# Optimization experiments

Measured on AMD Instinct MI355X. Metric: run time of the kernel, lower is better.

The kernel has to match this reference:

```python
import jax, jax.numpy as jnp
import numpy as np

QK_I2_S = 128  # elements per packed block (32 bytes -> 128 2-bit weights)


def unpack_weights_simd(packed):
    """Unpack SIMD block-interleaved 2-bit ternary weights.

    packed: (M, K//4) int values in [0, 256). Per 32-byte block, byte j holds
    weights at offsets j+0 (bits 6:7), j+32 (bits 4:5), j+64 (bits 2:3), j+96 (bits 0:1).
    Returns float32 (M, K) with values in {-1, 0, 1, 2}-1 = {-1,0,1,2}? (2-bit code minus 1).
    """
    M, Kp = packed.shape
    nb = Kp // 32                      # number of 128-element blocks
    p = packed.reshape(M, nb, 32)
    shifts = jnp.array([6, 4, 2, 0], dtype=jnp.int32)
    # (M, nb, 4, 32): axis 2 indexes the offset group {0,32,64,96}
    w = ((p[:, :, None, :] >> shifts[None, None, :, None]) & 3).astype(jnp.float32) - 1.0
    return w.reshape(M, nb * QK_I2_S)  # (M, K)


def quantize_activations_i8(x):
    """Per-token symmetric int8 quantization (absmax -> [-128, 127])."""
    absmax = jnp.max(jnp.abs(x), axis=-1, keepdims=True)
    q_scale = 127.0 / jnp.clip(absmax, 1e-5, None)   # x_i8 = round(x * q_scale)
    x_i8 = jnp.clip(jnp.round(x * q_scale), -128.0, 127.0)
    act_scale = 1.0 / q_scale                         # dequant scale = absmax/127
    return x_i8, act_scale


def setup_inputs() -> dict:
    key = jax.random.key(0)
    k1, k2, k3 = jax.random.split(key, 3)
    x = jax.random.normal(k1, (2, 2048, 4096), dtype=jnp.float32)
    weight = jax.random.randint(k2, (12288, 1024), 0, 256, dtype=jnp.int32)
    weight_scale = jax.random.uniform(k3, (1,), dtype=jnp.float32, minval=0.01, maxval=0.1)
    return {"x": x, "weight": weight, "weight_scale": weight_scale}


def reference(x, weight, weight_scale):
    orig_shape = x.shape[:-1]
    K = x.shape[-1]
    x_flat = x.reshape(-1, K).astype(jnp.float32)
    x_i8, act_scale = quantize_activations_i8(x_flat)      # (N,K), (N,1)
    W = unpack_weights_simd(weight)                         # (M,K) ternary-coded floats
    # bitnet_gemm: int8 activations x ternary weights, fused weight scale
    out = jnp.einsum('nk,mk->nm', x_i8, W) * weight_scale[0]
    out = (out * act_scale).astype(x.dtype)                 # dequantize activations
    return out.reshape(*orig_shape, -1)
```

## Files before the change

kernel.cpp:

```cpp
#include <hip/hip_runtime.h>

#define K_DIM 4096
#define M_DIM 12288
#define KW (K_DIM / 4)
#define NT_K (K_DIM / 128)
#define BM 256
#define BN 256
#define GN 16
#define GM 48

typedef __attribute__((ext_vector_type(4))) int i32x4;
typedef __attribute__((ext_vector_type(4))) unsigned int u32x4;

__device__ __forceinline__ int quant1(float v, float qs) {
  float r = rintf(v * qs);
  r = fminf(127.f, fmaxf(-128.f, r));
  return (int)r;
}

__device__ __forceinline__ unsigned int unp(unsigned int uv) {
  return ((uv >> 6) | (uv << 4) | (uv << 14) | (uv << 24)) & 0x03030303u;
}

__global__ __launch_bounds__(256) void quant_kernel(const float* __restrict__ x,
                                                    unsigned int* __restrict__ xq,
                                                    float2* __restrict__ scales) {
  const int n = blockIdx.x;
  const int t = threadIdx.x;
  const float* __restrict__ row = x + (size_t)n * K_DIM;
  const float4* __restrict__ row4 = (const float4*)row;

  float am = 0.f;
#pragma unroll
  for (int p = 0; p < 4; ++p) {
    float4 v = row4[t + 256 * p];
    am = fmaxf(am, fmaxf(fmaxf(fabsf(v.x), fabsf(v.y)), fmaxf(fabsf(v.z), fabsf(v.w))));
  }
#pragma unroll
  for (int off = 32; off; off >>= 1) am = fmaxf(am, __shfl_xor(am, off, 64));
  __shared__ float redf[4];
  __shared__ int redi[4];
  const int wave = t >> 6, lane = t & 63;
  if (lane == 0) redf[wave] = am;
  __syncthreads();
  am = fmaxf(fmaxf(redf[0], redf[1]), fmaxf(redf[2], redf[3]));
  const float clipped = fmaxf(am, 1e-5f);
  const float qs = 127.0f / clipped;

  int rsum = 0;
#pragma unroll
  for (int p = 0; p < 4; ++p) {
    const int w = t + 256 * p;
    const int b = w >> 5, j = w & 31;
    const int base = b * 128 + j;
    const int q0 = quant1(row[base], qs);
    const int q1 = quant1(row[base + 32], qs);
    const int q2 = quant1(row[base + 64], qs);
    const int q3 = quant1(row[base + 96], qs);
    rsum += q0 + q1 + q2 + q3;
    xq[(size_t)n * KW + w] = (unsigned int)(q0 & 255) | ((unsigned int)(q1 & 255) << 8) |
                             ((unsigned int)(q2 & 255) << 16) | ((unsigned int)(q3 & 255) << 24);
  }
#pragma unroll
  for (int off = 32; off; off >>= 1) rsum += __shfl_xor(rsum, off, 64);
  if (lane == 0) redi[wave] = rsum;
  __syncthreads();
  if (t == 0)
    scales[n] = make_float2(clipped * (1.0f / 127.0f),
                            (float)(redi[0] + redi[1] + redi[2] + redi[3]));
}

__global__ __launch_bounds__(256) void unpack_kernel(const i32x4* __restrict__ in,
                                                     u32x4* __restrict__ outp, int n4) {
  int idx = blockIdx.x * 256 + threadIdx.x;
  const int stride = gridDim.x * 256;
  for (; idx < n4; idx += stride) {
    i32x4 v = in[idx];
    u32x4 u = {unp((unsigned int)v[0]), unp((unsigned int)v[1]),
               unp((unsigned int)v[2]), unp((unsigned int)v[3])};
    outp[idx] = u;
  }
}

template <bool PRE>
__global__ __launch_bounds__(512) void bitgemm256(const unsigned char* __restrict__ xq,
                                                  const unsigned char* __restrict__ wu,
                                                  const int* __restrict__ wp,
                                                  const float2* __restrict__ scales,
                                                  const float* __restrict__ wsp,
                                                  float* __restrict__ out) {
  __shared__ __align__(16) unsigned char lds[131072];
  unsigned char* AsB = lds;
  unsigned char* BsB = lds + 65536;

  const int tid = threadIdx.x;
  const int l = tid & 63;
  const int w = tid >> 6;
  const int wm = w >> 2;
  const int wn = w & 3;

  const int cpx = gridDim.x >> 3;
  const int swz = (blockIdx.x & 7) * cpx + (blockIdx.x >> 3);
  const int bn = swz & (GN - 1);
  const int bm = swz >> 4;

  const int srow = tid >> 3;
  const int schunk = (tid & 7) ^ (srow & 7);
  const size_t soff = (size_t)srow * K_DIM + (schunk << 4);
  const unsigned char* aSrc = xq + (size_t)(bn * BM) * K_DIM + soff;
  const unsigned char* bSrc = wu + (size_t)(bm * BN) * K_DIM + soff;
  const int ldsDst = tid * 16;

  const int prow = tid >> 1, phalf = tid & 1;
  const int* pSrc = wp + (size_t)(bm * BN + prow) * KW + phalf * 16;
  const int pchunkbase = phalf * 4;
  const int pswz = prow & 7;
  const int pdst = prow * 128;

  int aoff[8], boff[4];
#pragma unroll
  for (int i = 0; i < 8; ++i) {
    const int r = wm * 128 + i * 16 + (l & 15);
    aoff[i] = r * 128 + (((l >> 4) ^ (r & 7)) << 4);
  }
#pragma unroll
  for (int j = 0; j < 4; ++j) {
    const int r = wn * 64 + j * 16 + (l & 15);
    boff[j] = r * 128 + (((l >> 4) ^ (r & 7)) << 4);
  }

  i32x4 acc[8][4];
#pragma unroll
  for (int i = 0; i < 8; ++i)
#pragma unroll
    for (int j = 0; j < 4; ++j) acc[i][j] = (i32x4){0, 0, 0, 0};

  auto stage = [&](int buf, int kb) {
    const int koff = kb * 128;
    unsigned char* ad = AsB + buf * 32768 + ldsDst;
    const unsigned char* as_ = aSrc + koff;
#pragma unroll
    for (int q = 0; q < 4; ++q)
      __builtin_amdgcn_global_load_lds(
          (const __attribute__((address_space(1))) void*)(as_ + (size_t)q * 64 * K_DIM),
          (__attribute__((address_space(3))) void*)(ad + q * 8192), 16, 0, 0);
    if (PRE) {
      unsigned char* bd = BsB + buf * 32768 + ldsDst;
      const unsigned char* bs_ = bSrc + koff;
#pragma unroll
      for (int q = 0; q < 4; ++q)
        __builtin_amdgcn_global_load_lds(
            (const __attribute__((address_space(1))) void*)(bs_ + (size_t)q * 64 * K_DIM),
            (__attribute__((address_space(3))) void*)(bd + q * 8192), 16, 0, 0);
    } else {
      const int* ps = pSrc + kb * 32;
      unsigned char* bd = BsB + buf * 32768 + pdst;
#pragma unroll
      for (int q = 0; q < 4; ++q) {
        i32x4 v = *(const i32x4*)(ps + q * 4);
        u32x4 u = {unp((unsigned int)v[0]), unp((unsigned int)v[1]),
                   unp((unsigned int)v[2]), unp((unsigned int)v[3])};
        *(u32x4*)(bd + (((pchunkbase + q) ^ pswz) << 4)) = u;
      }
    }
  };

  stage(0, 0);
  for (int kb = 0; kb < NT_K; ++kb) {
    const int cur = kb & 1;
    if (kb + 1 < NT_K) {
      stage(cur ^ 1, kb + 1);
      asm volatile("s_waitcnt vmcnt(8)" ::: "memory");
    } else {
      asm volatile("s_waitcnt vmcnt(0)" ::: "memory");
    }
    __builtin_amdgcn_s_barrier();

    const unsigned char* Ab = AsB + cur * 32768;
    const unsigned char* Bb = BsB + cur * 32768;
#pragma unroll
    for (int ks = 0; ks < 2; ++ks) {
      const int k6 = ks << 6;
      i32x4 af[8], bf[4];
#pragma unroll
      for (int i = 0; i < 8; ++i) af[i] = *(const i32x4*)(Ab + (aoff[i] ^ k6));
#pragma unroll
      for (int j = 0; j < 4; ++j) bf[j] = *(const i32x4*)(Bb + (boff[j] ^ k6));
      __builtin_amdgcn_s_setprio(1);
#pragma unroll
      for (int i = 0; i < 8; ++i)
#pragma unroll
        for (int j = 0; j < 4; ++j)
          acc[i][j] = __builtin_amdgcn_mfma_i32_16x16x64_i8(af[i], bf[j], acc[i][j], 0, 0, 0);
      __builtin_amdgcn_s_setprio(0);
    }
    if (!PRE) asm volatile("s_waitcnt lgkmcnt(0)" ::: "memory");
    __builtin_amdgcn_s_barrier();
  }

  const float wsc = wsp[0];
#pragma unroll
  for (int i = 0; i < 8; ++i) {
#pragma unroll
    for (int r = 0; r < 4; ++r) {
      const int n = bn * BM + wm * 128 + i * 16 + ((l >> 4) << 2) + r;
      const float2 sc = scales[n];
      const float f = wsc * sc.x;
      float* orow = out + (size_t)n * M_DIM + bm * BN + wn * 64 + (l & 15);
#pragma unroll
      for (int j = 0; j < 4; ++j) orow[j * 16] = ((float)acc[i][j][r] - sc.y) * f;
    }
  }
}

extern "C" void kernel_launch(void* const* d_in, const int* in_sizes, int n_in,
                              void* d_out, int out_size, void* d_ws, size_t ws_size,
                              hipStream_t stream) {
  const float* x = (const float*)d_in[0];
  const int* wp = (const int*)d_in[1];
  const float* wsp = (const float*)d_in[2];
  float* out = (float*)d_out;
  const int N = in_sizes[0] / K_DIM;

  float2* scales = (float2*)d_ws;
  unsigned int* xq = (unsigned int*)((char*)d_ws + 32768);
  const size_t xq_bytes = (size_t)N * KW * 4;
  unsigned char* wu = (unsigned char*)d_ws + 32768 + xq_bytes;
  const size_t need = 32768 + xq_bytes + (size_t)M_DIM * K_DIM;

  quant_kernel<<<N, 256, 0, stream>>>(x, xq, scales);
  const int grid = (N / BM) * GM;
  if (ws_size >= need) {
    unpack_kernel<<<2048, 256, 0, stream>>>((const i32x4*)wp, (u32x4*)wu, M_DIM * KW / 4);
    bitgemm256<true><<<grid, 512, 0, stream>>>((const unsigned char*)xq, wu, wp, scales, wsp, out);
  } else {
    bitgemm256<false><<<grid, 512, 0, stream>>>((const unsigned char*)xq, nullptr, wp, scales, wsp, out);
  }
}
```

Baseline: 237.6 us.

## Pre-tile unpacked weights in MFMA fragment order and load B directly to registers

Measured after the change: 254.9 us. 7.3% more time.

```diff
diff --git a/kernel.cpp b/kernel.cpp
--- a/kernel.cpp
+++ b/kernel.cpp
@@ -70,28 +70,53 @@
                             (float)(redi[0] + redi[1] + redi[2] + redi[3]));
 }
 
-__global__ __launch_bounds__(256) void unpack_kernel(const i32x4* __restrict__ in,
-                                                     u32x4* __restrict__ outp, int n4) {
-  int idx = blockIdx.x * 256 + threadIdx.x;
+__global__ __launch_bounds__(256) void unpack_tiled(const int* __restrict__ in,
+                                                    u32x4* __restrict__ outp) {
+  const int total = M_DIM * 256;
+  int t = blockIdx.x * 256 + threadIdx.x;
   const int stride = gridDim.x * 256;
-  for (; idx < n4; idx += stride) {
-    i32x4 v = in[idx];
-    u32x4 u = {unp((unsigned int)v[0]), unp((unsigned int)v[1]),
-               unp((unsigned int)v[2]), unp((unsigned int)v[3])};
-    outp[idx] = u;
-  }
-}
-
-template <bool PRE>
-__global__ __launch_bounds__(512) void bitgemm256(const unsigned char* __restrict__ xq,
-                                                  const unsigned char* __restrict__ wu,
-                                                  const int* __restrict__ wp,
-                                                  const float2* __restrict__ scales,
-                                                  const float* __restrict__ wsp,
-                                                  float* __restrict__ out) {
-  __shared__ __align__(16) unsigned char lds[131072];
-  unsigned char* AsB = lds;
-  unsigned char* BsB = lds + 65536;
+  for (; t < total; t += stride) {
+    const int lo = t & 15;
+    const int cc = (t >> 4) & 255;
+    const int rt = t >> 12;
+    const int r = rt * 16 + lo;
+    const i32x4 v = *(const i32x4*)(in + (size_t)r * KW + cc * 4);
+    u32x4 u = {unp((unsigned int)v[0]), unp((unsigned int)v[1]), unp((unsigned int)v[2]),
+               unp((unsigned int)v[3])};
+    const int kb = cc >> 3, c8 = cc & 7;
+    outp[rt * 4096 + kb * 128 + (c8 >> 2) * 64 + (c8 & 3) * 16 + lo] = u;
+  }
+}
+
+#define LOAD_B(dst, kb)                                                                   \
+  {                                                                                       \
+    _Pragma("unroll") for (int q_ = 0; q_ < 8; ++q_) dst[q_] =                            \
+        *(const i32x4*)(bBase + (q_ & 3) * 65536 + (q_ >> 2) * 1024 + (size_t)(kb) * 2048); \
+  }
+
+#define COMPUTE(Ab, bS)                                                                   \
+  {                                                                                       \
+    _Pragma("unroll") for (int ih_ = 0; ih_ < 2; ++ih_) {                                 \
+      _Pragma("unroll") for (int ks_ = 0; ks_ < 2; ++ks_) {                               \
+        i32x4 af[4];                                                                      \
+        _Pragma("unroll") for (int i_ = 0; i_ < 4; ++i_) af[i_] =                         \
+            *(const i32x4*)((Ab) + (aoff[ih_ * 4 + i_] ^ (ks_ << 6)));                    \
+        __builtin_amdgcn_s_setprio(1);                                                    \
+        _Pragma("unroll") for (int i_ = 0; i_ < 4; ++i_)                                  \
+            _Pragma("unroll") for (int j_ = 0; j_ < 4; ++j_) acc[ih_ * 4 + i_][j_] =      \
+                __builtin_amdgcn_mfma_i32_16x16x64_i8(af[i_], bS[ks_ * 4 + j_],           \
+                                                      acc[ih_ * 4 + i_][j_], 0, 0, 0);    \
+        __builtin_amdgcn_s_setprio(0);                                                    \
+      }                                                                                   \
+    }                                                                                     \
+  }
+
+__global__ __launch_bounds__(512, 2) void bitgemm256(const unsigned char* __restrict__ xq,
+                                                     const unsigned char* __restrict__ wu2,
+                                                     const float2* __restrict__ scales,
+                                                     const float* __restrict__ wsp,
+                                                     float* __restrict__ out) {
+  __shared__ __align__(16) unsigned char lds[65536];
 
   const int tid = threadIdx.x;
   const int l = tid & 63;
@@ -106,28 +131,17 @@
 
   const int srow = tid >> 3;
   const int schunk = (tid & 7) ^ (srow & 7);
-  const size_t soff = (size_t)srow * K_DIM + (schunk << 4);
-  const unsigned char* aSrc = xq + (size_t)(bn * BM) * K_DIM + soff;
-  const unsigned char* bSrc = wu + (size_t)(bm * BN) * K_DIM + soff;
+  const unsigned char* aSrc = xq + (size_t)(bn * BM) * K_DIM + (size_t)srow * K_DIM + (schunk << 4);
   const int ldsDst = tid * 16;
 
-  const int prow = tid >> 1, phalf = tid & 1;
-  const int* pSrc = wp + (size_t)(bm * BN + prow) * KW + phalf * 16;
-  const int pchunkbase = phalf * 4;
-  const int pswz = prow & 7;
-  const int pdst = prow * 128;
-
-  int aoff[8], boff[4];
+  const unsigned char* bBase = wu2 + (((size_t)(bm * 16 + wn * 4) * 4096 + l) << 4);
+
+  int aoff[8];
 #pragma unroll
   for (int i = 0; i < 8; ++i) {
     const int r = wm * 128 + i * 16 + (l & 15);
     aoff[i] = r * 128 + (((l >> 4) ^ (r & 7)) << 4);
   }
-#pragma unroll
-  for (int j = 0; j < 4; ++j) {
-    const int r = wn * 64 + j * 16 + (l & 15);
-    boff[j] = r * 128 + (((l >> 4) ^ (r & 7)) << 4);
-  }
 
   i32x4 acc[8][4];
 #pragma unroll
@@ -135,66 +149,39 @@
 #pragma unroll
     for (int j = 0; j < 4; ++j) acc[i][j] = (i32x4){0, 0, 0, 0};
 
-  auto stage = [&](int buf, int kb) {
-    const int koff = kb * 128;
-    unsigned char* ad = AsB + buf * 32768 + ldsDst;
-    const unsigned char* as_ = aSrc + koff;
+  auto stageA = [&](int buf, int kb) {
+    unsigned char* ad = lds + buf * 32768 + ldsDst;
+    const unsigned char* as_ = aSrc + kb * 128;
 #pragma unroll
     for (int q = 0; q < 4; ++q)
       __builtin_amdgcn_global_load_lds(
           (const __attribute__((address_space(1))) void*)(as_ + (size_t)q * 64 * K_DIM),
           (__attribute__((address_space(3))) void*)(ad + q * 8192), 16, 0, 0);
-    if (PRE) {
-      unsigned char* bd = BsB + buf * 32768 + ldsDst;
-      const unsigned char* bs_ = bSrc + koff;
-#pragma unroll
-      for (int q = 0; q < 4; ++q)
-        __builtin_amdgcn_global_load_lds(
-            (const __attribute__((address_space(1))) void*)(bs_ + (size_t)q * 64 * K_DIM),
-            (__attribute__((address_space(3))) void*)(bd + q * 8192), 16, 0, 0);
-    } else {
-      const int* ps = pSrc + kb * 32;
-      unsigned char* bd = BsB + buf * 32768 + pdst;
-#pragma unroll
-      for (int q = 0; q < 4; ++q) {
-        i32x4 v = *(const i32x4*)(ps + q * 4);
-        u32x4 u = {unp((unsigned int)v[0]), unp((unsigned int)v[1]),
-                   unp((unsigned int)v[2]), unp((unsigned int)v[3])};
-        *(u32x4*)(bd + (((pchunkbase + q) ^ pswz) << 4)) = u;
-      }
-    }
   };
 
-  stage(0, 0);
-  for (int kb = 0; kb < NT_K; ++kb) {
-    const int cur = kb & 1;
-    if (kb + 1 < NT_K) {
-      stage(cur ^ 1, kb + 1);
-      asm volatile("s_waitcnt vmcnt(8)" ::: "memory");
+  i32x4 bX[8], bY[8];
+  const unsigned char* A0 = lds;
+  const unsigned char* A1 = lds + 32768;
+
+  stageA(0, 0);
+  LOAD_B(bX, 0);
+  for (int kb2 = 0; kb2 < NT_K / 2; ++kb2) {
+    const int e = kb2 * 2;
+    stageA(1, e + 1);
+    LOAD_B(bY, e + 1);
+    asm volatile("s_waitcnt vmcnt(12)" ::: "memory");
+    __builtin_amdgcn_s_barrier();
+    COMPUTE(A0, bX);
+    __builtin_amdgcn_s_barrier();
+    if (kb2 < NT_K / 2 - 1) {
+      stageA(0, e + 2);
+      LOAD_B(bX, e + 2);
+      asm volatile("s_waitcnt vmcnt(12)" ::: "memory");
     } else {
       asm volatile("s_waitcnt vmcnt(0)" ::: "memory");
     }
     __builtin_amdgcn_s_barrier();
-
-    const unsigned char* Ab = AsB + cur * 32768;
-    const unsigned char* Bb = BsB + cur * 32768;
-#pragma unroll
-    for (int ks = 0; ks < 2; ++ks) {
-      const int k6 = ks << 6;
-      i32x4 af[8], bf[4];
-#pragma unroll
-      for (int i = 0; i < 8; ++i) af[i] = *(const i32x4*)(Ab + (aoff[i] ^ k6));
-#pragma unroll
-      for (int j = 0; j < 4; ++j) bf[j] = *(const i32x4*)(Bb + (boff[j] ^ k6));
-      __builtin_amdgcn_s_setprio(1);
-#pragma unroll
-      for (int i = 0; i < 8; ++i)
-#pragma unroll
-        for (int j = 0; j < 4; ++j)
-          acc[i][j] = __builtin_amdgcn_mfma_i32_16x16x64_i8(af[i], bf[j], acc[i][j], 0, 0, 0);
-      __builtin_amdgcn_s_setprio(0);
-    }
-    if (!PRE) asm volatile("s_waitcnt lgkmcnt(0)" ::: "memory");
+    COMPUTE(A1, bY);
     __builtin_amdgcn_s_barrier();
   }
 
@@ -225,15 +212,10 @@
   float2* scales = (float2*)d_ws;
   unsigned int* xq = (unsigned int*)((char*)d_ws + 32768);
   const size_t xq_bytes = (size_t)N * KW * 4;
-  unsigned char* wu = (unsigned char*)d_ws + 32768 + xq_bytes;
-  const size_t need = 32768 + xq_bytes + (size_t)M_DIM * K_DIM;
+  unsigned char* wu2 = (unsigned char*)d_ws + 32768 + xq_bytes;
 
   quant_kernel<<<N, 256, 0, stream>>>(x, xq, scales);
+  unpack_tiled<<<4096, 256, 0, stream>>>(wp, (u32x4*)wu2);
   const int grid = (N / BM) * GM;
-  if (ws_size >= need) {
-    unpack_kernel<<<2048, 256, 0, stream>>>((const i32x4*)wp, (u32x4*)wu, M_DIM * KW / 4);
-    bitgemm256<true><<<grid, 512, 0, stream>>>((const unsigned char*)xq, wu, wp, scales, wsp, out);
-  } else {
-    bitgemm256<false><<<grid, 512, 0, stream>>>((const unsigned char*)xq, nullptr, wp, scales, wsp, out);
-  }
-}
+  bitgemm256<<<grid, 512, 0, stream>>>((const unsigned char*)xq, wu2, scales, wsp, out);
+}
```

## Switch GEMM to 128x128 tiles with 4 waves and two blocks per CU

Applied to the files above, without the earlier changes.

After: 308.8 us. 30.0% more time.

```diff
diff --git a/kernel.cpp b/kernel.cpp
--- a/kernel.cpp
+++ b/kernel.cpp
@@ -4,10 +4,9 @@
 #define M_DIM 12288
 #define KW (K_DIM / 4)
 #define NT_K (K_DIM / 128)
-#define BM 256
-#define BN 256
-#define GN 16
-#define GM 48
+#define BT 128
+#define GN2 32
+#define GM2 96
 
 typedef __attribute__((ext_vector_type(4))) int i32x4;
 typedef __attribute__((ext_vector_type(4))) unsigned int u32x4;
@@ -82,86 +81,59 @@
   }
 }
 
-template <bool PRE>
-__global__ __launch_bounds__(512) void bitgemm256(const unsigned char* __restrict__ xq,
-                                                  const unsigned char* __restrict__ wu,
-                                                  const int* __restrict__ wp,
-                                                  const float2* __restrict__ scales,
-                                                  const float* __restrict__ wsp,
-                                                  float* __restrict__ out) {
-  __shared__ __align__(16) unsigned char lds[131072];
-  unsigned char* AsB = lds;
-  unsigned char* BsB = lds + 65536;
+__global__ __launch_bounds__(256, 2) void bitgemm128(const unsigned char* __restrict__ xq,
+                                                     const unsigned char* __restrict__ wu,
+                                                     const float2* __restrict__ scales,
+                                                     const float* __restrict__ wsp,
+                                                     float* __restrict__ out) {
+  __shared__ __align__(16) unsigned char lds[65536];
 
   const int tid = threadIdx.x;
   const int l = tid & 63;
   const int w = tid >> 6;
-  const int wm = w >> 2;
-  const int wn = w & 3;
+  const int wm = w >> 1;
+  const int wn = w & 1;
 
   const int cpx = gridDim.x >> 3;
   const int swz = (blockIdx.x & 7) * cpx + (blockIdx.x >> 3);
-  const int bn = swz & (GN - 1);
-  const int bm = swz >> 4;
+  const int bn = swz / GM2;
+  const int bm = swz % GM2;
 
   const int srow = tid >> 3;
   const int schunk = (tid & 7) ^ (srow & 7);
   const size_t soff = (size_t)srow * K_DIM + (schunk << 4);
-  const unsigned char* aSrc = xq + (size_t)(bn * BM) * K_DIM + soff;
-  const unsigned char* bSrc = wu + (size_t)(bm * BN) * K_DIM + soff;
+  const unsigned char* aSrc = xq + (size_t)(bn * BT) * K_DIM + soff;
+  const unsigned char* bSrc = wu + (size_t)(bm * BT) * K_DIM + soff;
   const int ldsDst = tid * 16;
 
-  const int prow = tid >> 1, phalf = tid & 1;
-  const int* pSrc = wp + (size_t)(bm * BN + prow) * KW + phalf * 16;
-  const int pchunkbase = phalf * 4;
-  const int pswz = prow & 7;
-  const int pdst = prow * 128;
-
-  int aoff[8], boff[4];
-#pragma unroll
-  for (int i = 0; i < 8; ++i) {
-    const int r = wm * 128 + i * 16 + (l & 15);
-    aoff[i] = r * 128 + (((l >> 4) ^ (r & 7)) << 4);
-  }
-#pragma unroll
-  for (int j = 0; j < 4; ++j) {
-    const int r = wn * 64 + j * 16 + (l & 15);
-    boff[j] = r * 128 + (((l >> 4) ^ (r & 7)) << 4);
-  }
-
-  i32x4 acc[8][4];
-#pragma unroll
-  for (int i = 0; i < 8; ++i)
+  int aoff[4], boff[4];
+#pragma unroll
+  for (int i = 0; i < 4; ++i) {
+    const int ra = wm * 64 + i * 16 + (l & 15);
+    aoff[i] = ra * 128 + (((l >> 4) ^ (ra & 7)) << 4);
+    const int rb = wn * 64 + i * 16 + (l & 15);
+    boff[i] = rb * 128 + (((l >> 4) ^ (rb & 7)) << 4);
+  }
+
+  i32x4 acc[4][4];
+#pragma unroll
+  for (int i = 0; i < 4; ++i)
 #pragma unroll
     for (int j = 0; j < 4; ++j) acc[i][j] = (i32x4){0, 0, 0, 0};
 
   auto stage = [&](int buf, int kb) {
-    const int koff = kb * 128;
-    unsigned char* ad = AsB + buf * 32768 + ldsDst;
-    const unsigned char* as_ = aSrc + koff;
-#pragma unroll
-    for (int q = 0; q < 4; ++q)
+    unsigned char* ad = lds + buf * 16384 + ldsDst;
+    unsigned char* bd = lds + 32768 + buf * 16384 + ldsDst;
+    const unsigned char* as_ = aSrc + kb * 128;
+    const unsigned char* bs_ = bSrc + kb * 128;
+#pragma unroll
+    for (int q = 0; q < 4; ++q) {
       __builtin_amdgcn_global_load_lds(
-          (const __attribute__((address_space(1))) void*)(as_ + (size_t)q * 64 * K_DIM),
-          (__attribute__((address_space(3))) void*)(ad + q * 8192), 16, 0, 0);
-    if (PRE) {
-      unsigned char* bd = BsB + buf * 32768 + ldsDst;
-      const unsigned char* bs_ = bSrc + koff;
-#pragma unroll
-      for (int q = 0; q < 4; ++q)
-        __builtin_amdgcn_global_load_lds(
-            (const __attribute__((address_space(1))) void*)(bs_ + (size_t)q * 64 * K_DIM),
-            (__attribute__((address_space(3))) void*)(bd + q * 8192), 16, 0, 0);
-    } else {
-      const int* ps = pSrc + kb * 32;
-      unsigned char* bd = BsB + buf * 32768 + pdst;
-#pragma unroll
-      for (int q = 0; q < 4; ++q) {
-        i32x4 v = *(const i32x4*)(ps + q * 4);
-        u32x4 u = {unp((unsigned int)v[0]), unp((unsigned int)v[1]),
-                   unp((unsigned int)v[2]), unp((unsigned int)v[3])};
-        *(u32x4*)(bd + (((pchunkbase + q) ^ pswz) << 4)) = u;
-      }
+          (const __attribute__((address_space(1))) void*)(as_ + (size_t)q * 32 * K_DIM),
+          (__attribute__((address_space(3))) void*)(ad + q * 4096), 16, 0, 0);
+      __builtin_amdgcn_global_load_lds(
+          (const __attribute__((address_space(1))) void*)(bs_ + (size_t)q * 32 * K_DIM),
+          (__attribute__((address_space(3))) void*)(bd + q * 4096), 16, 0, 0);
     }
   };
 
@@ -176,37 +148,39 @@
     }
     __builtin_amdgcn_s_barrier();
 
-    const unsigned char* Ab = AsB + cur * 32768;
-    const unsigned char* Bb = BsB + cur * 32768;
+    const unsigned char* Ab = lds + cur * 16384;
+    const unsigned char* Bb = lds + 32768 + cur * 16384;
+    i32x4 af[8], bf[8];
 #pragma unroll
     for (int ks = 0; ks < 2; ++ks) {
-      const int k6 = ks << 6;
-      i32x4 af[8], bf[4];
-#pragma unroll
-      for (int i = 0; i < 8; ++i) af[i] = *(const i32x4*)(Ab + (aoff[i] ^ k6));
-#pragma unroll
-      for (int j = 0; j < 4; ++j) bf[j] = *(const i32x4*)(Bb + (boff[j] ^ k6));
-      __builtin_amdgcn_s_setprio(1);
-#pragma unroll
-      for (int i = 0; i < 8; ++i)
+#pragma unroll
+      for (int i = 0; i < 4; ++i) {
+        af[ks * 4 + i] = *(const i32x4*)(Ab + (aoff[i] ^ (ks << 6)));
+        bf[ks * 4 + i] = *(const i32x4*)(Bb + (boff[i] ^ (ks << 6)));
+      }
+    }
+    __builtin_amdgcn_s_setprio(1);
+#pragma unroll
+    for (int ks = 0; ks < 2; ++ks)
+#pragma unroll
+      for (int i = 0; i < 4; ++i)
 #pragma unroll
         for (int j = 0; j < 4; ++j)
-          acc[i][j] = __builtin_amdgcn_mfma_i32_16x16x64_i8(af[i], bf[j], acc[i][j], 0, 0, 0);
-      __builtin_amdgcn_s_setprio(0);
-    }
-    if (!PRE) asm volatile("s_waitcnt lgkmcnt(0)" ::: "memory");
+          acc[i][j] = __builtin_amdgcn_mfma_i32_16x16x64_i8(af[ks * 4 + i], bf[ks * 4 + j],
+                                                            acc[i][j], 0, 0, 0);
+    __builtin_amdgcn_s_setprio(0);
     __builtin_amdgcn_s_barrier();
   }
 
   const float wsc = wsp[0];
 #pragma unroll
-  for (int i = 0; i < 8; ++i) {
+  for (int i = 0; i < 4; ++i) {
 #pragma unroll
     for (int r = 0; r < 4; ++r) {
-      const int n = bn * BM + wm * 128 + i * 16 + ((l >> 4) << 2) + r;
+      const int n = bn * BT + wm * 64 + i * 16 + ((l >> 4) << 2) + r;
       const float2 sc = scales[n];
       const float f = wsc * sc.x;
-      float* orow = out + (size_t)n * M_DIM + bm * BN + wn * 64 + (l & 15);
+      float* orow = out + (size_t)n * M_DIM + bm * BT + wn * 64 + (l & 15);
 #pragma unroll
       for (int j = 0; j < 4; ++j) orow[j * 16] = ((float)acc[i][j][r] - sc.y) * f;
     }
@@ -226,14 +200,9 @@
   unsigned int* xq = (unsigned int*)((char*)d_ws + 32768);
   const size_t xq_bytes = (size_t)N * KW * 4;
   unsigned char* wu = (unsigned char*)d_ws + 32768 + xq_bytes;
-  const size_t need = 32768 + xq_bytes + (size_t)M_DIM * K_DIM;
 
   quant_kernel<<<N, 256, 0, stream>>>(x, xq, scales);
-  const int grid = (N / BM) * GM;
-  if (ws_size >= need) {
-    unpack_kernel<<<2048, 256, 0, stream>>>((const i32x4*)wp, (u32x4*)wu, M_DIM * KW / 4);
-    bitgemm256<true><<<grid, 512, 0, stream>>>((const unsigned char*)xq, wu, wp, scales, wsp, out);
-  } else {
-    bitgemm256<false><<<grid, 512, 0, stream>>>((const unsigned char*)xq, nullptr, wp, scales, wsp, out);
-  }
-}
+  unpack_kernel<<<2048, 256, 0, stream>>>((const i32x4*)wp, (u32x4*)wu, M_DIM * KW / 4);
+  const int grid = GN2 * GM2;
+  bitgemm128<<<grid, 256, 0, stream>>>((const unsigned char*)xq, wu, scales, wsp, out);
+}
```
